# Optimization experiments

Hardware: AMD Instinct MI355X
Metric: run time of the kernel (lower is better)

Reference implementation:

```python
import jax, jax.numpy as jnp
import numpy as np

B, S, D, M, NQ = 256, 200, 128, 64, 5000
A_TRI, B_TRI, C_TRI = 0.01, 0.05, 0.1  # triangular membership params a,b,c


def setup_inputs():
    key = jax.random.key(0)
    ks = jax.random.split(key, 16)
    g = lambda k, shp: jax.random.normal(k, shp, dtype=jnp.float32) * 0.05
    return dict(
        question_seq=jax.random.randint(ks[0], (B, S), 0, NQ),
        correctness_seq=jax.random.randint(ks[1], (B, S), 0, 2),
        Mk=g(ks[2], (M, D)),
        Mv0=g(ks[3], (M, D)),
        emb_concept=g(ks[4], (NQ, D)),
        emb_interaction=g(ks[5], (2 * NQ, D)),
        Wf=g(ks[6], (D, 2 * D)), bf=jnp.zeros((D,), jnp.float32),
        Wa=g(ks[7], (D, 2 * D)), ba=jnp.zeros((D,), jnp.float32),
        We=g(ks[8], (D, D)), be=jnp.zeros((D,), jnp.float32),
        Wadd=g(ks[9], (D, D)), badd=jnp.zeros((D,), jnp.float32),
        W_ih=g(ks[10], (4 * D, D)), W_hh=g(ks[11], (4 * D, D)),
        b_ih=jnp.zeros((4 * D,), jnp.float32), b_hh=jnp.zeros((4 * D,), jnp.float32),
        hx0=g(ks[12], (1, D)), cx0=g(ks[13], (1, D)),
        Wp=g(ks[14], (1, D)), bp=jnp.zeros((1,), jnp.float32),
    )


def _skvmn(Mk, Mv0, emb_concept, emb_interaction, Wf, bf, Wa, ba, We, be,
           Wadd, badd, W_ih, W_hh, b_ih, b_hh, hx0, cx0, Wp, bp,
           question_seq, correctness_seq):
    concept = emb_concept[question_seq]                                # [B,S,D]
    inter = emb_interaction[question_seq + NQ * correctness_seq]        # [B,S,D]

    # ---- DKVMN key addressing + value memory read/erase/add recurrence ----
    def mem_step(mem, xs):
        k_t, y_t = xs                                                   # [B,D]
        cw = jax.nn.softmax(k_t @ Mk.T, axis=1)                         # [B,M]
        read = jnp.einsum('bm,bmd->bd', cw, mem)                        # [B,D]
        f = jnp.tanh(jnp.concatenate([read, k_t], 1) @ Wf.T + bf)       # [B,D]
        we = jnp.concatenate([f, y_t], 1) @ Wa.T + ba                   # write embed
        erase = jax.nn.sigmoid(we @ We.T + be)
        add = jnp.tanh(we @ Wadd.T + badd)
        mem = mem * (1.0 - cw[:, :, None] * erase[:, None, :]) \
              + cw[:, :, None] * add[:, None, :]
        return mem, (cw, f)

    mem0 = jnp.broadcast_to(Mv0[None], (B, M, D)).astype(jnp.float32)
    _, (w, ft) = jax.lax.scan(
        mem_step, mem0,
        (concept.transpose(1, 0, 2), inter.transpose(1, 0, 2)))
    # w: [S,B,M], ft: [S,B,D]

    # ---- triangular layer: bin correlation weights into identity vectors ----
    wb = w.transpose(1, 0, 2)                                           # [B,S,M]
    tri = jnp.minimum((wb - A_TRI) / (B_TRI - A_TRI),
                      (C_TRI - wb) / (C_TRI - B_TRI))
    tri = jnp.maximum(tri, 0.0)
    iv = jnp.where(tri >= 0.6, 2.0, jnp.where(tri >= 0.1, 1.0, 0.0))    # [B,S,M]

    sq = jnp.sum(iv * iv, axis=2)                                       # [B,S]
    dist = sq[:, :, None] + sq[:, None, :] - 2.0 * jnp.einsum('btm,bjm->btj', iv, iv)
    NEG = jnp.float32(-1e32)
    d2 = jnp.where(dist > 0.0, NEG, dist)
    triu = jnp.triu(jnp.ones((S, S), bool), k=0)                        # mask j >= t
    d2 = jnp.where(triu[None], NEG, d2)
    idx_mat = jnp.arange(S * S, dtype=jnp.float32).reshape(S, S)
    score = d2 + idx_mat[None]                                          # [B,S,S]
    prev_t = jnp.argmax(score, axis=2)                                  # [B,S] prior matching step
    valid = jnp.max(score, axis=2) >= 0.0                               # [B,S]

    # ---- hop-LSTM: substitute hx with hidden state of prior matching step ----
    def lstm_step(carry, xs):
        hx, cx, H = carry
        t, x_t, prev_b, valid_b = xs
        h_prev = H[prev_b, jnp.arange(B)]                               # gather [B,D]
        hx = jnp.where(valid_b[:, None], h_prev, hx)
        gates = x_t @ W_ih.T + b_ih + hx @ W_hh.T + b_hh
        i_, f_, g_, o_ = jnp.split(gates, 4, axis=1)
        cx = jax.nn.sigmoid(f_) * cx + jax.nn.sigmoid(i_) * jnp.tanh(g_)
        hx = jax.nn.sigmoid(o_) * jnp.tanh(cx)
        H = jax.lax.dynamic_update_slice(H, hx[None], (t, 0, 0))
        return (hx, cx, H), hx

    H0 = jnp.zeros((S, B, D), jnp.float32)
    hx = jnp.broadcast_to(hx0, (B, D)).astype(jnp.float32)
    cx = jnp.broadcast_to(cx0, (B, D)).astype(jnp.float32)
    _, hs = jax.lax.scan(lstm_step, (hx, cx, H0),
                         (jnp.arange(S), ft, prev_t.T, valid.T))         # hs: [S,B,D]

    logits = jnp.einsum('sbd,d->sb', hs, Wp[0]) + bp[0]
    return jax.nn.sigmoid(logits).T                                     # [B,S]


def reference(question_seq, correctness_seq, Mk, Mv0, emb_concept, emb_interaction,
              Wf, bf, Wa, ba, We, be, Wadd, badd, W_ih, W_hh, b_ih, b_hh,
              hx0, cx0, Wp, bp):
    return _skvmn(Mk, Mv0, emb_concept, emb_interaction, Wf, bf, Wa, ba, We, be,
                  Wadd, badd, W_ih, W_hh, b_ih, b_hh, hx0, cx0, Wp, bp,
                  question_seq, correctness_seq)
```

## Files before the change

### kernel.cpp

```cpp
#include <hip/hip_runtime.h>

typedef unsigned int u32;
typedef unsigned short u16;
typedef unsigned long long u64;
typedef _Float16 f16;
typedef _Float16 f16x2 __attribute__((ext_vector_type(2)));

#define Bn 256
#define Sn 200
#define Dn 128
#define Mn 64
#define NQn 5000

__device__ __forceinline__ float fdot2f(u32 w, u32 x, float acc) {
#if __has_builtin(__builtin_amdgcn_fdot2)
    return __builtin_amdgcn_fdot2(__builtin_bit_cast(f16x2, w),
                                  __builtin_bit_cast(f16x2, x), acc, false);
#else
    f16x2 a = __builtin_bit_cast(f16x2, w);
    f16x2 b = __builtin_bit_cast(f16x2, x);
    return acc + (float)a[0] * (float)b[0] + (float)a[1] * (float)b[1];
#endif
}

__device__ __forceinline__ u32 packh2(float a, float b) {
    u16 ua = __builtin_bit_cast(u16, (f16)a);
    u16 ub = __builtin_bit_cast(u16, (f16)b);
    return (u32)ua | ((u32)ub << 16);
}

__device__ __forceinline__ float h2f(u16 u) { return (float)__builtin_bit_cast(f16, u); }

__device__ __forceinline__ float fexp2f(float x) {
#if __has_builtin(__builtin_amdgcn_exp2f)
    return __builtin_amdgcn_exp2f(x);
#else
    return exp2f(x);
#endif
}
__device__ __forceinline__ float frcpf(float x) {
#if __has_builtin(__builtin_amdgcn_rcpf)
    return __builtin_amdgcn_rcpf(x);
#else
    return 1.0f / x;
#endif
}
__device__ __forceinline__ float sig_fast(float x)  { return frcpf(1.0f + fexp2f(-1.44269504f * x)); }
__device__ __forceinline__ float tanh_fast(float x) { return fmaf(-2.0f, frcpf(1.0f + fexp2f(2.88539008f * x)), 1.0f); }

__global__ __launch_bounds__(512) void phase0_kernel(
    const int* __restrict__ qseq,
    const float* __restrict__ Mk, const float* __restrict__ embc,
    u16* __restrict__ cw16, ulonglong2* __restrict__ codes)
{
    __shared__ float MkT[Dn * 65];
    __shared__ float kb[8][Dn];
    int tid = threadIdx.x;
    for (int idx = tid; idx < Mn * Dn; idx += 512) {
        int m = idx >> 7, d = idx & 127;
        MkT[d * 65 + m] = Mk[idx];
    }
    __syncthreads();
    int w = tid >> 6, lane = tid & 63;
    int item = blockIdx.x * 8 + w;
    int qq = qseq[item];
    kb[w][lane]      = embc[qq * Dn + lane];
    kb[w][lane + 64] = embc[qq * Dn + lane + 64];
    __syncthreads();
    float acc = 0.0f;
    const float* kw = kb[w];
#pragma unroll 8
    for (int d = 0; d < Dn; ++d)
        acc = fmaf(MkT[d * 65 + lane], kw[d], acc);
    float mx = acc;
    for (int off = 32; off; off >>= 1) mx = fmaxf(mx, __shfl_xor(mx, off));
    float e = expf(acc - mx);
    float sm = e;
    for (int off = 32; off; off >>= 1) sm += __shfl_xor(sm, off);
    float cw = e / sm;
    cw16[item * Mn + lane] = __builtin_bit_cast(u16, (f16)cw);
    float t1 = (cw - 0.01f) / (0.05f - 0.01f);
    float t2 = (0.1f - cw) / (0.1f - 0.05f);
    float tri = fminf(t1, t2);
    tri = fmaxf(tri, 0.0f);
    int iv = (tri >= 0.6f) ? 2 : ((tri >= 0.1f) ? 1 : 0);
    u64 b1 = __ballot(iv >= 1);
    u64 b2 = __ballot(iv == 2);
    if (lane == 0) { codes[item].x = b1; codes[item].y = b2; }
}

__global__ __launch_bounds__(256) void match_kernel(
    const ulonglong2* __restrict__ codes, int* __restrict__ prev)
{
    __shared__ u64 clo[Sn], chi[Sn];
    int b = blockIdx.x, tid = threadIdx.x;
    if (tid < Sn) { ulonglong2 c = codes[b * Sn + tid]; clo[tid] = c.x; chi[tid] = c.y; }
    __syncthreads();
    if (tid < Sn) {
        u64 mylo = clo[tid], myhi = chi[tid];
        int best = -1;
        for (int j = 0; j < tid; ++j)
            if (clo[j] == mylo && chi[j] == myhi) best = j;
        prev[b * Sn + tid] = best;
    }
}

__global__ __launch_bounds__(512) void setup_kernel(
    const float* __restrict__ Wa, const float* __restrict__ We,
    const float* __restrict__ Wadd,
    const float* __restrict__ ba, const float* __restrict__ be,
    const float* __restrict__ badd,
    float* __restrict__ CEf, float* __restrict__ CAf,
    float* __restrict__ CEy, float* __restrict__ CAy,
    float* __restrict__ c0s)
{
    __shared__ float weR[128], waR[128];
    int d = blockIdx.x, tid = threadIdx.x;
    if (tid < 128) weR[tid] = We[d * 128 + tid];
    else if (tid < 256) waR[tid - 128] = Wadd[d * 128 + (tid - 128)];
    __syncthreads();
    int mat = tid >> 7, j = tid & 127;
    const float* src = (mat == 0 || mat == 2) ? weR : waR;
    int col = (mat < 2) ? j : (128 + j);
    float acc = 0.0f;
    for (int k = 0; k < 128; ++k) acc = fmaf(src[k], Wa[k * 256 + col], acc);
    float* dst = (mat == 0) ? CEf : (mat == 1) ? CAf : (mat == 2) ? CEy : CAy;
    dst[d * 128 + j] = acc;
    if (tid == 0) {
        float a = 0.0f;
        for (int k = 0; k < 128; ++k) a = fmaf(weR[k], ba[k], a);
        c0s[d] = a + be[d];
    } else if (tid == 1) {
        float a = 0.0f;
        for (int k = 0; k < 128; ++k) a = fmaf(waR[k], ba[k], a);
        c0s[128 + d] = a + badd[d];
    }
}

__global__ __launch_bounds__(512) void rowk_kernel(
    const float* __restrict__ W, const float* __restrict__ emb,
    u16* __restrict__ outp)
{
    __shared__ u32 wL[128 * 65];
    __shared__ u32 vb[8][64];
    int tid = threadIdx.x;
    for (int idx = tid; idx < 128 * 64; idx += 512) {
        int dd = idx >> 6, jj = idx & 63;
        const float2 wv = *(const float2*)(W + dd * 256 + 128 + 2 * jj);
        wL[dd * 65 + jj] = packh2(wv.x, wv.y);
    }
    int w = tid >> 6, lane = tid & 63;
    int row = blockIdx.x * 8 + w;
    {
        const float2 kv = *(const float2*)(emb + row * Dn + 2 * lane);
        vb[w][lane] = packh2(kv.x, kv.y);
    }
    __syncthreads();
    const u32* w0 = wL + lane * 65;
    const u32* w1 = wL + (64 + lane) * 65;
    const u32* x  = vb[w];
    float a0 = 0, a1 = 0, b0 = 0, b1 = 0;
#pragma unroll
    for (int jj = 0; jj < 64; jj += 2) {
        a0 = fdot2f(w0[jj],     x[jj],     a0);
        a1 = fdot2f(w0[jj + 1], x[jj + 1], a1);
        b0 = fdot2f(w1[jj],     x[jj],     b0);
        b1 = fdot2f(w1[jj + 1], x[jj + 1], b1);
    }
    outp[row * Dn + lane]      = __builtin_bit_cast(u16, (f16)(a0 + a1));
    outp[row * Dn + 64 + lane] = __builtin_bit_cast(u16, (f16)(b0 + b1));
}

__global__ __launch_bounds__(512) void rowe_kernel(
    const float* __restrict__ CEy, const float* __restrict__ CAy,
    const float* __restrict__ c0s, const float* __restrict__ embi,
    u16* __restrict__ ebR, u16* __restrict__ abR)
{
    __shared__ u32 eL[128 * 65];
    __shared__ u32 aL[128 * 65];
    __shared__ u32 vb[8][64];
    __shared__ float c0L[256];
    int tid = threadIdx.x;
    for (int idx = tid; idx < 128 * 64; idx += 512) {
        int dd = idx >> 6, jj = idx & 63;
        const float2 e2 = *(const float2*)(CEy + dd * 128 + 2 * jj);
        const float2 a2 = *(const float2*)(CAy + dd * 128 + 2 * jj);
        eL[dd * 65 + jj] = packh2(e2.x, e2.y);
        aL[dd * 65 + jj] = packh2(a2.x, a2.y);
    }
    if (tid < 256) c0L[tid] = c0s[tid];
    int w = tid >> 6, lane = tid & 63;
    int row = blockIdx.x * 8 + w;
    {
        const float2 kv = *(const float2*)(embi + row * Dn + 2 * lane);
        vb[w][lane] = packh2(kv.x, kv.y);
    }
    __syncthreads();
    const u32* x   = vb[w];
    const u32* e0p = eL + lane * 65;
    const u32* e1p = eL + (64 + lane) * 65;
    const u32* a0p = aL + lane * 65;
    const u32* a1p = aL + (64 + lane) * 65;
    float ea0 = 0, ea1 = 0, eb0 = 0, eb1 = 0;
    float aa0 = 0, aa1 = 0, ab0 = 0, ab1 = 0;
#pragma unroll
    for (int jj = 0; jj < 64; jj += 2) {
        ea0 = fdot2f(e0p[jj],     x[jj],     ea0);
        ea1 = fdot2f(e0p[jj + 1], x[jj + 1], ea1);
        eb0 = fdot2f(e1p[jj],     x[jj],     eb0);
        eb1 = fdot2f(e1p[jj + 1], x[jj + 1], eb1);
        aa0 = fdot2f(a0p[jj],     x[jj],     aa0);
        aa1 = fdot2f(a0p[jj + 1], x[jj + 1], aa1);
        ab0 = fdot2f(a1p[jj],     x[jj],     ab0);
        ab1 = fdot2f(a1p[jj + 1], x[jj + 1], ab1);
    }
    ebR[row * Dn + lane]      = __builtin_bit_cast(u16, (f16)(ea0 + ea1 + c0L[lane]));
    ebR[row * Dn + 64 + lane] = __builtin_bit_cast(u16, (f16)(eb0 + eb1 + c0L[64 + lane]));
    abR[row * Dn + lane]      = __builtin_bit_cast(u16, (f16)(aa0 + aa1 + c0L[128 + lane]));
    abR[row * Dn + 64 + lane] = __builtin_bit_cast(u16, (f16)(ab0 + ab1 + c0L[192 + lane]));
}

__global__ __launch_bounds__(512, 2) void memrec_kernel(
    const float* __restrict__ Mv0,
    const float* __restrict__ Wf, const float* __restrict__ bfv,
    const float* __restrict__ CEf, const float* __restrict__ CAf,
    const u16* __restrict__ cw16, const u16* __restrict__ kfR,
    const u16* __restrict__ ebR, const u16* __restrict__ abR,
    const int* __restrict__ qseq, const int* __restrict__ cseq,
    u16* __restrict__ ft16)
{
    __shared__ u32 cwL[Sn * 32];
    __shared__ __align__(16) u32 kfb[2][16 * 64];
    __shared__ __align__(16) u32 ebb[2][16 * 64];
    __shared__ __align__(16) u32 abb[2][16 * 64];
    __shared__ __align__(16) u32 rbuf[64], fbuf[64];
    __shared__ float bfL[Dn];
    __shared__ int qrowL[Sn], irowL[Sn];

    int tid = threadIdx.x;
    int d = tid >> 2, q = tid & 3;
    int b = blockIdx.x;

    u32 wfr[16], wew[16], wadw[16];
    {
        const float2* wf2 = (const float2*)(Wf  + d * 256 + q * 32);
        const float2* we2 = (const float2*)(CEf + d * 128 + q * 32);
        const float2* wd2 = (const float2*)(CAf + d * 128 + q * 32);
#pragma unroll
        for (int i = 0; i < 16; ++i) {
            float2 a;
            a = wf2[i]; wfr[i]  = packh2(a.x, a.y);
            a = we2[i]; wew[i]  = packh2(a.x, a.y);
            a = wd2[i]; wadw[i] = packh2(a.x, a.y);
        }
    }
    float memv[16];
#pragma unroll
    for (int i = 0; i < 16; ++i) memv[i] = Mv0[(q * 16 + i) * Dn + d];

    if (tid < Dn) bfL[tid] = bfv[tid];
    if (tid < Sn) {
        int qq = qseq[b * Sn + tid];
        qrowL[tid] = qq;
        irowL[tid] = qq + NQn * cseq[b * Sn + tid];
    }
    __syncthreads();

    for (int i = tid; i < Sn * 32; i += 512) cwL[i] = ((const u32*)cw16)[b * Sn * 32 + i];
    for (int i = tid; i < 1024; i += 512) {
        int s = i >> 6, off = i & 63;
        kfb[0][i] = ((const u32*)kfR)[qrowL[s] * 64 + off];
        ebb[0][i] = ((const u32*)ebR)[irowL[s] * 64 + off];
        abb[0][i] = ((const u32*)abR)[irowL[s] * 64 + off];
    }
    __syncthreads();

    float cwreg[16];
#pragma unroll
    for (int i = 0; i < 8; ++i) {
        u32 v = cwL[q * 8 + i];
        cwreg[2 * i]     = h2f((u16)(v & 0xffff));
        cwreg[2 * i + 1] = h2f((u16)(v >> 16));
    }

    for (int t = 0; t < Sn; ++t) {
        int sl = (t >> 4) & 1, ti = t & 15;
        if (ti == 0) {
            int c1 = (t >> 4) + 1;
            if (c1 * 16 < Sn) {
                int n = (Sn - c1 * 16 < 16 ? Sn - c1 * 16 : 16) * 64;
                for (int i = tid; i < n; i += 512) {
                    int s = i >> 6, off = i & 63;
                    int t2 = c1 * 16 + s;
                    kfb[sl ^ 1][i] = ((const u32*)kfR)[qrowL[t2] * 64 + off];
                    ebb[sl ^ 1][i] = ((const u32*)ebR)[irowL[t2] * 64 + off];
                    abb[sl ^ 1][i] = ((const u32*)abR)[irowL[t2] * 64 + off];
                }
            }
        }
        float p0 = 0, p1 = 0, p2 = 0, p3 = 0;
#pragma unroll
        for (int i = 0; i < 4; ++i) {
            p0 = fmaf(cwreg[i],      memv[i],      p0);
            p1 = fmaf(cwreg[4 + i],  memv[4 + i],  p1);
            p2 = fmaf(cwreg[8 + i],  memv[8 + i],  p2);
            p3 = fmaf(cwreg[12 + i], memv[12 + i], p3);
        }
        float pr = (p0 + p1) + (p2 + p3);
        pr += __shfl_xor(pr, 1);
        pr += __shfl_xor(pr, 2);
        if (q == 0) ((f16*)rbuf)[d] = (f16)pr;
        __syncthreads();
        u16 kfc = ((const u16*)(kfb[sl]))[ti * 128 + d];
        u16 ebc = ((const u16*)(ebb[sl]))[ti * 128 + d];
        u16 abc = ((const u16*)(abb[sl]))[ti * 128 + d];
        float a0 = 0, a1 = 0, a2 = 0, a3 = 0;
#pragma unroll
        for (int u = 0; u < 4; ++u) {
            uint4 x = ((const uint4*)rbuf)[(q << 2) + u];
            a0 = fdot2f(wfr[4 * u + 0], x.x, a0);
            a1 = fdot2f(wfr[4 * u + 1], x.y, a1);
            a2 = fdot2f(wfr[4 * u + 2], x.z, a2);
            a3 = fdot2f(wfr[4 * u + 3], x.w, a3);
        }
        float accf = (a0 + a1) + (a2 + a3);
        accf += __shfl_xor(accf, 1);
        accf += __shfl_xor(accf, 2);
        float fv = tanh_fast(accf + h2f(kfc) + bfL[d]);
        if (q == 0) ((f16*)fbuf)[d] = (f16)fv;
        if (q == 1) ft16[(size_t)(b * Sn + t) * Dn + d] = __builtin_bit_cast(u16, (f16)fv);
        __syncthreads();
        float e0 = 0, e1 = 0, g0 = 0, g1 = 0;
#pragma unroll
        for (int u = 0; u < 4; ++u) {
            uint4 x = ((const uint4*)fbuf)[(q << 2) + u];
            e0 = fdot2f(wew[4 * u + 0], x.x, e0);   g0 = fdot2f(wadw[4 * u + 0], x.x, g0);
            e1 = fdot2f(wew[4 * u + 1], x.y, e1);   g1 = fdot2f(wadw[4 * u + 1], x.y, g1);
            e0 = fdot2f(wew[4 * u + 2], x.z, e0);   g0 = fdot2f(wadw[4 * u + 2], x.z, g0);
            e1 = fdot2f(wew[4 * u + 3], x.w, e1);   g1 = fdot2f(wadw[4 * u + 3], x.w, g1);
        }
        float pe = e0 + e1, pa = g0 + g1;
        pe += __shfl_xor(pe, 1); pe += __shfl_xor(pe, 2);
        pa += __shfl_xor(pa, 1); pa += __shfl_xor(pa, 2);
        float ev = sig_fast(pe + h2f(ebc));
        float av = tanh_fast(pa + h2f(abc));
        u32 cwn[8];
        if (t + 1 < Sn) {
#pragma unroll
            for (int i = 0; i < 8; ++i) cwn[i] = cwL[(t + 1) * 32 + q * 8 + i];
        }
#pragma unroll
        for (int i = 0; i < 16; ++i) {
            float tt = fmaf(-ev, memv[i], av);
            memv[i] = fmaf(cwreg[i], tt, memv[i]);
        }
        if (t + 1 < Sn) {
#pragma unroll
            for (int i = 0; i < 8; ++i) {
                cwreg[2 * i]     = h2f((u16)(cwn[i] & 0xffff));
                cwreg[2 * i + 1] = h2f((u16)(cwn[i] >> 16));
            }
        }
    }
}

__global__ __launch_bounds__(512, 2) void lstm_kernel(
    const float* __restrict__ W_ih, const float* __restrict__ W_hh,
    const float* __restrict__ b_ih, const float* __restrict__ b_hh,
    const float* __restrict__ hx0, const float* __restrict__ cx0,
    const float* __restrict__ Wp, const float* __restrict__ bp,
    const u16* __restrict__ ft16, const int* __restrict__ prev,
    float* __restrict__ out)
{
    __shared__ __align__(16) u32 HL[(Sn + 1) * 64];
    __shared__ __align__(16) u32 ftb[2][16 * 64];
    __shared__ int prevL[Sn];
    __shared__ u32 wpL[64];
    __shared__ float bpL;

    int tid = threadIdx.x, b = blockIdx.x;
    int d = tid >> 2, q = tid & 3;
    u32 wx[4][16], wh[4][16];
    float bias[4];
#pragma unroll
    for (int g = 0; g < 4; ++g) {
        const float2* wi2 = (const float2*)(W_ih + (size_t)(g * 128 + d) * Dn + q * 32);
        const float2* wh2 = (const float2*)(W_hh + (size_t)(g * 128 + d) * Dn + q * 32);
#pragma unroll
        for (int i = 0; i < 16; ++i) {
            float2 a;
            a = wi2[i]; wx[g][i] = packh2(a.x, a.y);
            a = wh2[i]; wh[g][i] = packh2(a.x, a.y);
        }
        bias[g] = b_ih[g * 128 + d] + b_hh[g * 128 + d];
    }
    if (tid < 64) {
        HL[tid]  = packh2(hx0[2 * tid], hx0[2 * tid + 1]);
        wpL[tid] = packh2(Wp[2 * tid], Wp[2 * tid + 1]);
    }
    if (tid < Sn) prevL[tid] = prev[b * Sn + tid];
    if (tid == 0) bpL = bp[0];
    float cx = cx0[d];
    {
        const u32* fg = (const u32*)ft16 + (size_t)(b * Sn) * 64;
        for (int i = tid; i < 1024; i += 512) ftb[0][i] = fg[i];
    }
    __syncthreads();

    for (int t = 0; t < Sn; ++t) {
        int sl = (t >> 4) & 1, ti = t & 15;
        if (ti == 0) {
            int c1 = (t >> 4) + 1;
            if (c1 * 16 < Sn) {
                int n = (Sn - c1 * 16 < 16 ? Sn - c1 * 16 : 16) * 64;
                const u32* fg = (const u32*)ft16 + (size_t)(b * Sn + c1 * 16) * 64;
                for (int i = tid; i < n; i += 512) ftb[sl ^ 1][i] = fg[i];
            }
        }
        int pv = prevL[t];
        int hrow = (pv >= 0) ? (pv + 1) : t;
        const uint4* h4 = (const uint4*)(HL + hrow * 64 + q * 16);
        const uint4* f4 = (const uint4*)(ftb[sl] + ti * 64 + q * 16);
        uint4 xv[4], yv[4];
#pragma unroll
        for (int u = 0; u < 4; ++u) { xv[u] = f4[u]; yv[u] = h4[u]; }
        float gacc[4];
#pragma unroll
        for (int g = 0; g < 4; ++g) {
            float s0 = 0, s1 = 0, s2 = 0, s3 = 0;
#pragma unroll
            for (int u = 0; u < 4; ++u) {
                s0 = fdot2f(wx[g][4 * u + 0], xv[u].x, s0);
                s1 = fdot2f(wx[g][4 * u + 1], xv[u].y, s1);
                s2 = fdot2f(wx[g][4 * u + 2], xv[u].z, s2);
                s3 = fdot2f(wx[g][4 * u + 3], xv[u].w, s3);
                s0 = fdot2f(wh[g][4 * u + 0], yv[u].x, s0);
                s1 = fdot2f(wh[g][4 * u + 1], yv[u].y, s1);
                s2 = fdot2f(wh[g][4 * u + 2], yv[u].z, s2);
                s3 = fdot2f(wh[g][4 * u + 3], yv[u].w, s3);
            }
            float s = (s0 + s1) + (s2 + s3);
            s += __shfl_xor(s, 1);
            s += __shfl_xor(s, 2);
            gacc[g] = s + bias[g];
        }
        float ig = sig_fast(gacc[0]);
        float fgt = sig_fast(gacc[1]);
        float gg = tanh_fast(gacc[2]);
        float og = sig_fast(gacc[3]);
        cx = fmaf(fgt, cx, ig * gg);
        float h = og * tanh_fast(cx);
        if (q == 0) ((f16*)HL)[(t + 1) * Dn + d] = (f16)h;
        __syncthreads();
    }
    if (tid < Sn) {
        float acc = 0.0f;
        const u32* hr = HL + (tid + 1) * 64;
#pragma unroll 16
        for (int j = 0; j < 64; ++j) acc = fdot2f(hr[j], wpL[j], acc);
        out[b * Sn + tid] = sig_fast(acc + bpL);
    }
}

extern "C" void kernel_launch(void* const* d_in, const int* in_sizes, int n_in,
                              void* d_out, int out_size, void* d_ws, size_t ws_size,
                              hipStream_t stream) {
    const int*   qseq = (const int*)d_in[0];
    const int*   cseq = (const int*)d_in[1];
    const float* Mk   = (const float*)d_in[2];
    const float* Mv0  = (const float*)d_in[3];
    const float* embc = (const float*)d_in[4];
    const float* embi = (const float*)d_in[5];
    const float* Wf   = (const float*)d_in[6];
    const float* bfv  = (const float*)d_in[7];
    const float* Wa   = (const float*)d_in[8];
    const float* bav  = (const float*)d_in[9];
    const float* We   = (const float*)d_in[10];
    const float* bev  = (const float*)d_in[11];
    const float* Wadd = (const float*)d_in[12];
    const float* badv = (const float*)d_in[13];
    const float* W_ih = (const float*)d_in[14];
    const float* W_hh = (const float*)d_in[15];
    const float* b_ih = (const float*)d_in[16];
    const float* b_hh = (const float*)d_in[17];
    const float* hx0  = (const float*)d_in[18];
    const float* cx0  = (const float*)d_in[19];
    const float* Wp   = (const float*)d_in[20];
    const float* bp   = (const float*)d_in[21];
    float* out = (float*)d_out;

    char* ws = (char*)d_ws;
    u16* cw16 = (u16*)ws;
    u16* ft16 = (u16*)(ws + 6553600);
    ulonglong2* codes = (ulonglong2*)(ws + 19660800);
    int* prev = (int*)(ws + 20480000);
    u16* kfR  = (u16*)(ws + 20684800);
    u16* ebR  = (u16*)(ws + 21964800);
    u16* abR  = (u16*)(ws + 24524800);
    float* CEf = (float*)(ws + 27084800);
    float* CAf = (float*)(ws + 27150336);
    float* CEy = (float*)(ws + 27215872);
    float* CAy = (float*)(ws + 27281408);
    float* c0s = (float*)(ws + 27346944);

    setup_kernel<<<128, 512, 0, stream>>>(Wa, We, Wadd, bav, bev, badv,
                                          CEf, CAf, CEy, CAy, c0s);
    phase0_kernel<<<(Bn * Sn) / 8, 512, 0, stream>>>(qseq, Mk, embc, cw16, codes);
    rowk_kernel<<<NQn / 8, 512, 0, stream>>>(Wf, embc, kfR);
    rowe_kernel<<<(2 * NQn) / 8, 512, 0, stream>>>(CEy, CAy, c0s, embi, ebR, abR);
    match_kernel<<<Bn, 256, 0, stream>>>(codes, prev);
    memrec_kernel<<<Bn, 512, 0, stream>>>(Mv0, Wf, bfv, CEf, CAf,
                                          cw16, kfR, ebR, abR, qseq, cseq, ft16);
    lstm_kernel<<<Bn, 512, 0, stream>>>(W_ih, W_hh, b_ih, b_hh, hx0, cx0, Wp, bp,
                                        ft16, prev, out);
}
```

Baseline: 638.9 us.

## Fuse memory recurrence and LSTM recurrence into one per-batch kernel

Merges the memory read/erase/add recurrence kernel and the LSTM kernel into one kernel, so each timestep computes f_t and immediately feeds it into the LSTM gate computation. This removes the global round-trip of the ft16 intermediate and its double-buffered prefetch, one launch, and one serial 200-step pass. Both recurrences now share per-step barriers. The cost is much higher register pressure: Wf/We/Wadd fragments plus all W_ih/W_hh fragments stay resident under a 512-thread, 2-block launch bound, which risks spills or lower occupancy. It also rotates the final projection loop index per thread, which may reduce LDS bank conflicts.

```diff
diff --git a/kernel.cpp b/kernel.cpp
--- a/kernel.cpp
+++ b/kernel.cpp
@@ -220,22 +220,30 @@
     abR[row * Dn + 64 + lane] = __builtin_bit_cast(u16, (f16)(ab0 + ab1 + c0L[192 + lane]));
 }
 
-__global__ __launch_bounds__(512, 2) void memrec_kernel(
+__global__ __launch_bounds__(512, 2) void fused_kernel(
     const float* __restrict__ Mv0,
     const float* __restrict__ Wf, const float* __restrict__ bfv,
     const float* __restrict__ CEf, const float* __restrict__ CAf,
     const u16* __restrict__ cw16, const u16* __restrict__ kfR,
     const u16* __restrict__ ebR, const u16* __restrict__ abR,
     const int* __restrict__ qseq, const int* __restrict__ cseq,
-    u16* __restrict__ ft16)
+    const float* __restrict__ W_ih, const float* __restrict__ W_hh,
+    const float* __restrict__ b_ih, const float* __restrict__ b_hh,
+    const float* __restrict__ hx0, const float* __restrict__ cx0,
+    const float* __restrict__ Wp, const float* __restrict__ bp,
+    const int* __restrict__ prev,
+    float* __restrict__ out)
 {
     __shared__ u32 cwL[Sn * 32];
     __shared__ __align__(16) u32 kfb[2][16 * 64];
     __shared__ __align__(16) u32 ebb[2][16 * 64];
     __shared__ __align__(16) u32 abb[2][16 * 64];
     __shared__ __align__(16) u32 rbuf[64], fbuf[64];
+    __shared__ __align__(16) u32 HL[(Sn + 1) * 64];
     __shared__ float bfL[Dn];
-    __shared__ int qrowL[Sn], irowL[Sn];
+    __shared__ int qrowL[Sn], irowL[Sn], prevL[Sn];
+    __shared__ u32 wpL[64];
+    __shared__ float bpL;
 
     int tid = threadIdx.x;
     int d = tid >> 2, q = tid & 3;
@@ -254,15 +262,36 @@
             a = wd2[i]; wadw[i] = packh2(a.x, a.y);
         }
     }
+    u32 wx[4][16], wh[4][16];
+    float bias[4];
+#pragma unroll
+    for (int g = 0; g < 4; ++g) {
+        const float2* wi2 = (const float2*)(W_ih + (size_t)(g * 128 + d) * Dn + q * 32);
+        const float2* wh2 = (const float2*)(W_hh + (size_t)(g * 128 + d) * Dn + q * 32);
+#pragma unroll
+        for (int i = 0; i < 16; ++i) {
+            float2 a;
+            a = wi2[i]; wx[g][i] = packh2(a.x, a.y);
+            a = wh2[i]; wh[g][i] = packh2(a.x, a.y);
+        }
+        bias[g] = b_ih[g * 128 + d] + b_hh[g * 128 + d];
+    }
     float memv[16];
 #pragma unroll
     for (int i = 0; i < 16; ++i) memv[i] = Mv0[(q * 16 + i) * Dn + d];
+    float cx = cx0[d];
 
     if (tid < Dn) bfL[tid] = bfv[tid];
+    if (tid < 64) {
+        HL[tid]  = packh2(hx0[2 * tid], hx0[2 * tid + 1]);
+        wpL[tid] = packh2(Wp[2 * tid], Wp[2 * tid + 1]);
+    }
+    if (tid == 0) bpL = bp[0];
     if (tid < Sn) {
         int qq = qseq[b * Sn + tid];
         qrowL[tid] = qq;
         irowL[tid] = qq + NQn * cseq[b * Sn + tid];
+        prevL[tid] = prev[b * Sn + tid];
     }
     __syncthreads();
 
@@ -328,102 +357,29 @@
         accf += __shfl_xor(accf, 2);
         float fv = tanh_fast(accf + h2f(kfc) + bfL[d]);
         if (q == 0) ((f16*)fbuf)[d] = (f16)fv;
-        if (q == 1) ft16[(size_t)(b * Sn + t) * Dn + d] = __builtin_bit_cast(u16, (f16)fv);
         __syncthreads();
+        uint4 xv[4];
+#pragma unroll
+        for (int u = 0; u < 4; ++u) xv[u] = ((const uint4*)fbuf)[(q << 2) + u];
         float e0 = 0, e1 = 0, g0 = 0, g1 = 0;
 #pragma unroll
         for (int u = 0; u < 4; ++u) {
-            uint4 x = ((const uint4*)fbuf)[(q << 2) + u];
-            e0 = fdot2f(wew[4 * u + 0], x.x, e0);   g0 = fdot2f(wadw[4 * u + 0], x.x, g0);
-            e1 = fdot2f(wew[4 * u + 1], x.y, e1);   g1 = fdot2f(wadw[4 * u + 1], x.y, g1);
-            e0 = fdot2f(wew[4 * u + 2], x.z, e0);   g0 = fdot2f(wadw[4 * u + 2], x.z, g0);
-            e1 = fdot2f(wew[4 * u + 3], x.w, e1);   g1 = fdot2f(wadw[4 * u + 3], x.w, g1);
+            e0 = fdot2f(wew[4 * u + 0], xv[u].x, e0);   g0 = fdot2f(wadw[4 * u + 0], xv[u].x, g0);
+            e1 = fdot2f(wew[4 * u + 1], xv[u].y, e1);   g1 = fdot2f(wadw[4 * u + 1], xv[u].y, g1);
+            e0 = fdot2f(wew[4 * u + 2], xv[u].z, e0);   g0 = fdot2f(wadw[4 * u + 2], xv[u].z, g0);
+            e1 = fdot2f(wew[4 * u + 3], xv[u].w, e1);   g1 = fdot2f(wadw[4 * u + 3], xv[u].w, g1);
         }
         float pe = e0 + e1, pa = g0 + g1;
         pe += __shfl_xor(pe, 1); pe += __shfl_xor(pe, 2);
         pa += __shfl_xor(pa, 1); pa += __shfl_xor(pa, 2);
         float ev = sig_fast(pe + h2f(ebc));
         float av = tanh_fast(pa + h2f(abc));
-        u32 cwn[8];
-        if (t + 1 < Sn) {
-#pragma unroll
-            for (int i = 0; i < 8; ++i) cwn[i] = cwL[(t + 1) * 32 + q * 8 + i];
-        }
-#pragma unroll
-        for (int i = 0; i < 16; ++i) {
-            float tt = fmaf(-ev, memv[i], av);
-            memv[i] = fmaf(cwreg[i], tt, memv[i]);
-        }
-        if (t + 1 < Sn) {
-#pragma unroll
-            for (int i = 0; i < 8; ++i) {
-                cwreg[2 * i]     = h2f((u16)(cwn[i] & 0xffff));
-                cwreg[2 * i + 1] = h2f((u16)(cwn[i] >> 16));
-            }
-        }
-    }
-}
-
-__global__ __launch_bounds__(512, 2) void lstm_kernel(
-    const float* __restrict__ W_ih, const float* __restrict__ W_hh,
-    const float* __restrict__ b_ih, const float* __restrict__ b_hh,
-    const float* __restrict__ hx0, const float* __restrict__ cx0,
-    const float* __restrict__ Wp, const float* __restrict__ bp,
-    const u16* __restrict__ ft16, const int* __restrict__ prev,
-    float* __restrict__ out)
-{
-    __shared__ __align__(16) u32 HL[(Sn + 1) * 64];
-    __shared__ __align__(16) u32 ftb[2][16 * 64];
-    __shared__ int prevL[Sn];
-    __shared__ u32 wpL[64];
-    __shared__ float bpL;
-
-    int tid = threadIdx.x, b = blockIdx.x;
-    int d = tid >> 2, q = tid & 3;
-    u32 wx[4][16], wh[4][16];
-    float bias[4];
-#pragma unroll
-    for (int g = 0; g < 4; ++g) {
-        const float2* wi2 = (const float2*)(W_ih + (size_t)(g * 128 + d) * Dn + q * 32);
-        const float2* wh2 = (const float2*)(W_hh + (size_t)(g * 128 + d) * Dn + q * 32);
-#pragma unroll
-        for (int i = 0; i < 16; ++i) {
-            float2 a;
-            a = wi2[i]; wx[g][i] = packh2(a.x, a.y);
-            a = wh2[i]; wh[g][i] = packh2(a.x, a.y);
-        }
-        bias[g] = b_ih[g * 128 + d] + b_hh[g * 128 + d];
-    }
-    if (tid < 64) {
-        HL[tid]  = packh2(hx0[2 * tid], hx0[2 * tid + 1]);
-        wpL[tid] = packh2(Wp[2 * tid], Wp[2 * tid + 1]);
-    }
-    if (tid < Sn) prevL[tid] = prev[b * Sn + tid];
-    if (tid == 0) bpL = bp[0];
-    float cx = cx0[d];
-    {
-        const u32* fg = (const u32*)ft16 + (size_t)(b * Sn) * 64;
-        for (int i = tid; i < 1024; i += 512) ftb[0][i] = fg[i];
-    }
-    __syncthreads();
-
-    for (int t = 0; t < Sn; ++t) {
-        int sl = (t >> 4) & 1, ti = t & 15;
-        if (ti == 0) {
-            int c1 = (t >> 4) + 1;
-            if (c1 * 16 < Sn) {
-                int n = (Sn - c1 * 16 < 16 ? Sn - c1 * 16 : 16) * 64;
-                const u32* fg = (const u32*)ft16 + (size_t)(b * Sn + c1 * 16) * 64;
-                for (int i = tid; i < n; i += 512) ftb[sl ^ 1][i] = fg[i];
-            }
-        }
         int pv = prevL[t];
         int hrow = (pv >= 0) ? (pv + 1) : t;
         const uint4* h4 = (const uint4*)(HL + hrow * 64 + q * 16);
-        const uint4* f4 = (const uint4*)(ftb[sl] + ti * 64 + q * 16);
-        uint4 xv[4], yv[4];
-#pragma unroll
-        for (int u = 0; u < 4; ++u) { xv[u] = f4[u]; yv[u] = h4[u]; }
+        uint4 yv[4];
+#pragma unroll
+        for (int u = 0; u < 4; ++u) yv[u] = h4[u];
         float gacc[4];
 #pragma unroll
         for (int g = 0; g < 4; ++g) {
@@ -444,20 +400,40 @@
             s += __shfl_xor(s, 2);
             gacc[g] = s + bias[g];
         }
-        float ig = sig_fast(gacc[0]);
+        float ig  = sig_fast(gacc[0]);
         float fgt = sig_fast(gacc[1]);
-        float gg = tanh_fast(gacc[2]);
-        float og = sig_fast(gacc[3]);
+        float gg  = tanh_fast(gacc[2]);
+        float og  = sig_fast(gacc[3]);
         cx = fmaf(fgt, cx, ig * gg);
-        float h = og * tanh_fast(cx);
-        if (q == 0) ((f16*)HL)[(t + 1) * Dn + d] = (f16)h;
-        __syncthreads();
-    }
+        float hv = og * tanh_fast(cx);
+        if (q == 0) ((f16*)HL)[(t + 1) * Dn + d] = (f16)hv;
+        u32 cwn[8];
+        if (t + 1 < Sn) {
+#pragma unroll
+            for (int i = 0; i < 8; ++i) cwn[i] = cwL[(t + 1) * 32 + q * 8 + i];
+        }
+#pragma unroll
+        for (int i = 0; i < 16; ++i) {
+            float tt = fmaf(-ev, memv[i], av);
+            memv[i] = fmaf(cwreg[i], tt, memv[i]);
+        }
+        if (t + 1 < Sn) {
+#pragma unroll
+            for (int i = 0; i < 8; ++i) {
+                cwreg[2 * i]     = h2f((u16)(cwn[i] & 0xffff));
+                cwreg[2 * i + 1] = h2f((u16)(cwn[i] >> 16));
+            }
+        }
+    }
+    __syncthreads();
     if (tid < Sn) {
         float acc = 0.0f;
         const u32* hr = HL + (tid + 1) * 64;
-#pragma unroll 16
-        for (int j = 0; j < 64; ++j) acc = fdot2f(hr[j], wpL[j], acc);
+#pragma unroll 8
+        for (int j = 0; j < 64; ++j) {
+            int jj = (j + tid) & 63;
+            acc = fdot2f(hr[jj], wpL[jj], acc);
+        }
         out[b * Sn + tid] = sig_fast(acc + bpL);
     }
 }
@@ -491,17 +467,16 @@
 
     char* ws = (char*)d_ws;
     u16* cw16 = (u16*)ws;
-    u16* ft16 = (u16*)(ws + 6553600);
-    ulonglong2* codes = (ulonglong2*)(ws + 19660800);
-    int* prev = (int*)(ws + 20480000);
-    u16* kfR  = (u16*)(ws + 20684800);
-    u16* ebR  = (u16*)(ws + 21964800);
-    u16* abR  = (u16*)(ws + 24524800);
-    float* CEf = (float*)(ws + 27084800);
-    float* CAf = (float*)(ws + 27150336);
-    float* CEy = (float*)(ws + 27215872);
-    float* CAy = (float*)(ws + 27281408);
-    float* c0s = (float*)(ws + 27346944);
+    ulonglong2* codes = (ulonglong2*)(ws + 6553600);
+    int* prev = (int*)(ws + 7372800);
+    u16* kfR  = (u16*)(ws + 7577600);
+    u16* ebR  = (u16*)(ws + 8857600);
+    u16* abR  = (u16*)(ws + 11417600);
+    float* CEf = (float*)(ws + 13977600);
+    float* CAf = (float*)(ws + 14043136);
+    float* CEy = (float*)(ws + 14108672);
+    float* CAy = (float*)(ws + 14174208);
+    float* c0s = (float*)(ws + 14239744);
 
     setup_kernel<<<128, 512, 0, stream>>>(Wa, We, Wadd, bav, bev, badv,
                                           CEf, CAf, CEy, CAy, c0s);
@@ -509,8 +484,8 @@
     rowk_kernel<<<NQn / 8, 512, 0, stream>>>(Wf, embc, kfR);
     rowe_kernel<<<(2 * NQn) / 8, 512, 0, stream>>>(CEy, CAy, c0s, embi, ebR, abR);
     match_kernel<<<Bn, 256, 0, stream>>>(codes, prev);
-    memrec_kernel<<<Bn, 512, 0, stream>>>(Mv0, Wf, bfv, CEf, CAf,
-                                          cw16, kfR, ebR, abR, qseq, cseq, ft16);
-    lstm_kernel<<<Bn, 512, 0, stream>>>(W_ih, W_hh, b_ih, b_hh, hx0, cx0, Wp, bp,
-                                        ft16, prev, out);
-}
+    fused_kernel<<<Bn, 512, 0, stream>>>(Mv0, Wf, bfv, CEf, CAf,
+                                         cw16, kfR, ebR, abR, qseq, cseq,
+                                         W_ih, W_hh, b_ih, b_hh, hx0, cx0, Wp, bp,
+                                         prev, out);
+}
```

New measurement: 999.5 us. +56.4%, slower.
